# Optimization experiments

Hardware: AMD Instinct MI355X
Metric: run time of the kernel (lower is better)

Reference implementation:

```python
import jax, jax.numpy as jnp
import numpy as np

N_NODES = 1_000_000
N_UPD = 200_000
D_MEM = 172
D_MSG = 172


def setup_inputs() -> dict:
    key = jax.random.key(0)
    ks = jax.random.split(key, 8)
    memory = jax.random.normal(ks[0], (N_NODES, D_MEM), dtype=jnp.float32)
    last_update = jnp.zeros((N_NODES,), dtype=jnp.float32)
    # unique node ids (no duplicates, as guaranteed by the caller in the original code)
    unique_node_ids = jax.random.permutation(ks[1], N_NODES)[:N_UPD].astype(jnp.int64)
    unique_messages = jax.random.normal(ks[2], (N_UPD, D_MSG), dtype=jnp.float32)
    timestamps = jax.random.uniform(ks[3], (N_UPD,), dtype=jnp.float32) * 1e6
    s_ih = 1.0 / np.sqrt(D_MEM)
    weight_ih = jax.random.uniform(ks[4], (3 * D_MEM, D_MSG), jnp.float32, -s_ih, s_ih)
    weight_hh = jax.random.uniform(ks[5], (3 * D_MEM, D_MEM), jnp.float32, -s_ih, s_ih)
    bias_ih = jax.random.uniform(ks[6], (3 * D_MEM,), jnp.float32, -s_ih, s_ih)
    bias_hh = jax.random.uniform(ks[7], (3 * D_MEM,), jnp.float32, -s_ih, s_ih)
    return {
        "memory": memory,
        "last_update": last_update,
        "unique_node_ids": unique_node_ids,
        "unique_messages": unique_messages,
        "timestamps": timestamps,
        "weight_ih": weight_ih,
        "weight_hh": weight_hh,
        "bias_ih": bias_ih,
        "bias_hh": bias_hh,
    }


def _gru_cell(x, h, weight_ih, weight_hh, bias_ih, bias_hh):
    # PyTorch GRUCell, gate order: reset, update, new
    gi = x @ weight_ih.T + bias_ih          # [M, 3H]
    gh = h @ weight_hh.T + bias_hh          # [M, 3H]
    i_r, i_z, i_n = jnp.split(gi, 3, axis=-1)
    h_r, h_z, h_n = jnp.split(gh, 3, axis=-1)
    r = jax.nn.sigmoid(i_r + h_r)
    z = jax.nn.sigmoid(i_z + h_z)
    n = jnp.tanh(i_n + r * h_n)
    return n + z * (h - n)                  # (1-z)*n + z*h


def reference(memory, last_update, unique_node_ids, unique_messages, timestamps,
              weight_ih, weight_hh, bias_ih, bias_hh):
    # gather rows of the node memory for the updated nodes
    h = memory[unique_node_ids]                                   # [M, D]
    h_new = _gru_cell(unique_messages, h, weight_ih, weight_hh, bias_ih, bias_hh)
    # scatter updated rows back (ids are unique)
    updated_memory = memory.at[unique_node_ids].set(h_new)        # [N, D]
    updated_last_update = last_update.at[unique_node_ids].set(timestamps)
    # original module returns memory with the singleton middle dim restored
    return updated_memory[:, None, :], updated_last_update
```

## Files before the change

### kernel.cpp

```cpp
#include <hip/hip_runtime.h>

typedef __attribute__((ext_vector_type(8))) short short8;
typedef __attribute__((ext_vector_type(4))) float f32x4;

#define N_NODES 1000000
#define N_UPD   200000
#define D       172
#define BM      64
#define LDA     360
#define KSTEPS  11
#define NTILES  48
#define KSLICE  (NTILES*512)
#define GRU_BLOCKS (N_UPD / BM)
#define NM4 43000000
#define BPACK_USHORTS (KSTEPS*KSLICE)
#define BIAS_OFF  (BPACK_USHORTS*2)
#define MASK_OFF  (BIAS_OFF + 688*4)
#define WS_NEED   (MASK_OFF + N_NODES)

__device__ __forceinline__ unsigned short f2bf(float f) {
  union { float f; unsigned u; } v; v.f = f;
  unsigned r = v.u + 0x7FFFu + ((v.u >> 16) & 1u);
  return (unsigned short)(r >> 16);
}
__device__ __forceinline__ float bf2f(unsigned short h) {
  union { unsigned u; float f; } v; v.u = ((unsigned)h) << 16;
  return v.f;
}
__device__ __forceinline__ ushort4 f2bf4(float4 v) {
  return make_ushort4(f2bf(v.x), f2bf(v.y), f2bf(v.z), f2bf(v.w));
}

__global__ void prep_kernel(const float* __restrict__ wih, const float* __restrict__ whh,
                            const float* __restrict__ bih, const float* __restrict__ bhh,
                            unsigned short* __restrict__ Bpack, float* __restrict__ bias4,
                            uint4* __restrict__ mask16) {
  int gid = blockIdx.x * 256 + threadIdx.x;
  if (gid < 688) {
    int which = gid / 172, j = gid % 172;
    float v;
    if (which == 0)      v = bih[j]       + bhh[j];
    else if (which == 1) v = bih[172 + j] + bhh[172 + j];
    else if (which == 2) v = bih[344 + j];
    else                 v = bhh[344 + j];
    bias4[gid] = v;
  }
  if (gid < N_NODES / 16) mask16[gid] = make_uint4(0, 0, 0, 0);
  if (gid >= BPACK_USHORTS) return;
  int e  = gid & 7;
  int l  = (gid >> 3) & 63;
  int nt = (gid >> 9) % NTILES;
  int ks = gid / KSLICE;
  int k  = ks * 32 + ((l >> 4) << 3) + e;
  int c  = l & 15;
  int w  = nt / 12, tl = nt % 12;
  int gate = tl / 3, ti = tl % 3;
  int j = w * 48 + ti * 16 + c;
  float v = 0.f;
  if (j < D) {
    if (gate == 0) {
      if (k < D)        v = wih[j * D + k];
      else if (k < 2*D) v = whh[j * D + (k - D)];
    } else if (gate == 1) {
      if (k < D)        v = wih[(D + j) * D + k];
      else if (k < 2*D) v = whh[(D + j) * D + (k - D)];
    } else if (gate == 2) {
      if (k < D)        v = wih[(2*D + j) * D + k];
    } else {
      if (k >= D && k < 2*D) v = whh[(2*D + j) * D + (k - D)];
    }
  }
  Bpack[gid] = f2bf(v);
}

__global__ void mask_set_kernel(const int* __restrict__ ids, unsigned char* __restrict__ mask) {
  int i = blockIdx.x * 256 + threadIdx.x;
  if (i < N_UPD) mask[ids[i]] = 1;
}

__global__ void copy_kernel(const float4* __restrict__ mem4, const float4* __restrict__ lu4,
                            float4* __restrict__ out4, float4* __restrict__ outlu4) {
  const long NL4 = N_NODES / 4;
  long stride = (long)gridDim.x * blockDim.x;
  for (long i = (long)blockIdx.x * blockDim.x + threadIdx.x; i < NM4 + NL4; i += stride) {
    if (i < NM4) out4[i] = mem4[i];
    else         outlu4[i - NM4] = lu4[i - NM4];
  }
}

__global__ __launch_bounds__(256)
void copy_masked_kernel(const float4* __restrict__ mem4, const float* __restrict__ lu,
                        const unsigned char* __restrict__ mask,
                        float4* __restrict__ out4, float* __restrict__ outlu) {
  const unsigned stride = gridDim.x * 256;
  for (unsigned i = blockIdx.x * 256 + threadIdx.x; i < NM4; i += stride) {
    unsigned row = i / 43u;
    if (!mask[row]) out4[i] = mem4[i];
  }
  for (unsigned j = blockIdx.x * 256 + threadIdx.x; j < N_NODES; j += stride) {
    if (!mask[j]) outlu[j] = lu[j];
  }
}

__global__ __launch_bounds__(512, 4)
void gru64_kernel(const float* __restrict__ memory, const float* __restrict__ msgs,
                  const int* __restrict__ ids, const float* __restrict__ ts,
                  const unsigned short* __restrict__ Bpack, const float* __restrict__ bias4,
                  float* __restrict__ out_mem, float* __restrict__ out_lu) {
  __shared__ unsigned short At[BM * LDA];
  const int tid  = threadIdx.x;
  const int m0   = blockIdx.x * BM;
  const int wave = tid >> 6, lane = tid & 63;
  const int g = lane >> 4, c = lane & 15;
  const int wm = wave >> 2, wc = wave & 3;

  const float4* x4 = (const float4*)msgs + (size_t)m0 * 43;
  float4 xv[6], hv[6];
  #pragma unroll
  for (int i = 0; i < 6; ++i) {
    int s = tid + i * 512;
    if (i < 5 || s < 2752) xv[i] = x4[s];
  }
  #pragma unroll
  for (int i = 0; i < 6; ++i) {
    int s = tid + i * 512;
    if (i < 5 || s < 2752) {
      int row = s / 43, seg = s - row * 43;
      hv[i] = ((const float4*)(memory + (size_t)ids[m0 + row] * D))[seg];
    }
  }
  #pragma unroll
  for (int i = 0; i < 6; ++i) {
    int s = tid + i * 512;
    if (i < 5 || s < 2752) {
      int row = s / 43, seg = s - row * 43;
      *(ushort4*)&At[row * LDA + seg * 4]       = f2bf4(xv[i]);
      *(ushort4*)&At[row * LDA + 172 + seg * 4] = f2bf4(hv[i]);
    }
  }
  if (tid < BM) {
    *(uint4*)&At[tid * LDA + 344] = make_uint4(0, 0, 0, 0);
    out_lu[ids[m0 + tid]] = ts[m0 + tid];
  }
  __syncthreads();

  const int ar0 = (wm * 32 + c) * LDA;
  const int ar1 = ar0 + 16 * LDA;
  const short8* Bp = (const short8*)Bpack;

  #pragma unroll 1
  for (int ti = 0; ti < 3; ++ti) {
    if (wc == 3 && ti == 2) continue;
    const short8* bp = Bp + (size_t)((wc * 12 + ti) * 64 + lane);

    f32x4 Cr0={0,0,0,0}, Cr1={0,0,0,0};
    f32x4 Cz0={0,0,0,0}, Cz1={0,0,0,0};
    f32x4 Ci0={0,0,0,0}, Ci1={0,0,0,0};
    f32x4 Ch0={0,0,0,0}, Ch1={0,0,0,0};

    #pragma unroll 2
    for (int ks = 0; ks < KSTEPS; ++ks) {
      const short8* bk = bp + ks * 3072;
      short8 br = bk[0];
      short8 bz = bk[192];
      short8 bi = bk[384];
      short8 bh = bk[576];
      short8 a0 = *(const short8*)&At[ar0 + ks * 32 + g * 8];
      short8 a1 = *(const short8*)&At[ar1 + ks * 32 + g * 8];
      Cr0 = __builtin_amdgcn_mfma_f32_16x16x32_bf16(a0, br, Cr0, 0, 0, 0);
      Cr1 = __builtin_amdgcn_mfma_f32_16x16x32_bf16(a1, br, Cr1, 0, 0, 0);
      Cz0 = __builtin_amdgcn_mfma_f32_16x16x32_bf16(a0, bz, Cz0, 0, 0, 0);
      Cz1 = __builtin_amdgcn_mfma_f32_16x16x32_bf16(a1, bz, Cz1, 0, 0, 0);
      Ci0 = __builtin_amdgcn_mfma_f32_16x16x32_bf16(a0, bi, Ci0, 0, 0, 0);
      Ci1 = __builtin_amdgcn_mfma_f32_16x16x32_bf16(a1, bi, Ci1, 0, 0, 0);
      Ch0 = __builtin_amdgcn_mfma_f32_16x16x32_bf16(a0, bh, Ch0, 0, 0, 0);
      Ch1 = __builtin_amdgcn_mfma_f32_16x16x32_bf16(a1, bh, Ch1, 0, 0, 0);
    }

    const int j = wc * 48 + ti * 16 + c;
    if (j < D) {
      const float b_r = bias4[j];
      const float b_z = bias4[172 + j];
      const float b_i = bias4[344 + j];
      const float b_h = bias4[516 + j];
      #pragma unroll
      for (int r = 0; r < 4; ++r) {
        {
          const int row_local = wm * 32 + g * 4 + r;
          float* orow = out_mem + (size_t)ids[m0 + row_local] * D;
          float ho = bf2f(At[row_local * LDA + 172 + j]);
          float rr = 1.f / (1.f + __expf(-(Cr0[r] + b_r)));
          float zz = 1.f / (1.f + __expf(-(Cz0[r] + b_z)));
          float e2 = __expf(2.f * (Ci0[r] + b_i + rr * (Ch0[r] + b_h)));
          float nn = 1.f - 2.f / (e2 + 1.f);
          orow[j] = nn + zz * (ho - nn);
        }
        {
          const int row_local = wm * 32 + 16 + g * 4 + r;
          float* orow = out_mem + (size_t)ids[m0 + row_local] * D;
          float ho = bf2f(At[row_local * LDA + 172 + j]);
          float rr = 1.f / (1.f + __expf(-(Cr1[r] + b_r)));
          float zz = 1.f / (1.f + __expf(-(Cz1[r] + b_z)));
          float e2 = __expf(2.f * (Ci1[r] + b_i + rr * (Ch1[r] + b_h)));
          float nn = 1.f - 2.f / (e2 + 1.f);
          orow[j] = nn + zz * (ho - nn);
        }
      }
    }
  }
}

extern "C" void kernel_launch(void* const* d_in, const int* in_sizes, int n_in,
                              void* d_out, int out_size, void* d_ws, size_t ws_size,
                              hipStream_t stream) {
  const float* memory      = (const float*)d_in[0];
  const float* last_update = (const float*)d_in[1];
  const int*   ids         = (const int*)  d_in[2];
  const float* msgs        = (const float*)d_in[3];
  const float* ts          = (const float*)d_in[4];
  const float* wih         = (const float*)d_in[5];
  const float* whh         = (const float*)d_in[6];
  const float* bih         = (const float*)d_in[7];
  const float* bhh         = (const float*)d_in[8];

  float* out_mem = (float*)d_out;
  float* out_lu  = out_mem + (size_t)N_NODES * D;

  unsigned short* Bpack = (unsigned short*)d_ws;
  float* bias4 = (float*)((char*)d_ws + BIAS_OFF);
  unsigned char* mask = (unsigned char*)d_ws + MASK_OFF;

  prep_kernel<<<BPACK_USHORTS / 256, 256, 0, stream>>>(wih, whh, bih, bhh, Bpack, bias4,
                                                       (uint4*)mask);
  if (ws_size >= WS_NEED) {
    mask_set_kernel<<<(N_UPD + 255) / 256, 256, 0, stream>>>(ids, mask);
    copy_masked_kernel<<<2048, 256, 0, stream>>>((const float4*)memory, last_update, mask,
                                                 (float4*)out_mem, out_lu);
  } else {
    copy_kernel<<<4096, 256, 0, stream>>>((const float4*)memory, (const float4*)last_update,
                                          (float4*)out_mem, (float4*)out_lu);
  }
  gru64_kernel<<<GRU_BLOCKS, 512, 0, stream>>>(memory, msgs, ids, ts, Bpack, bias4,
                                               out_mem, out_lu);
}
```

Before: 492.7 us.

## Interleave packed B weights per lane, software-pipeline B loads, row-coalesced A staging

The packed weight layout is reordered so each lane's four gate fragments for a k-step sit contiguously, and the GRU kernel's k-loop is fully unrolled with a three-stage register prefetch of B fragments ahead of the MFMAs. The A-tile staging now has 8 threads per row load contiguous float4s from message and memory rows, which gives contiguous access within each gathered row. Bf16 conversion switches to the HIP library paired round-to-nearest intrinsic. The aim is to hide weight-load latency and improve gather coalescing, at the cost of more live registers under the 512x4 launch bound.

```diff
diff --git a/kernel.cpp b/kernel.cpp
--- a/kernel.cpp
+++ b/kernel.cpp
@@ -1,4 +1,5 @@
 #include <hip/hip_runtime.h>
+#include <hip/hip_bf16.h>
 
 typedef __attribute__((ext_vector_type(8))) short short8;
 typedef __attribute__((ext_vector_type(4))) float f32x4;
@@ -9,26 +10,24 @@
 #define BM      64
 #define LDA     360
 #define KSTEPS  11
-#define NTILES  48
-#define KSLICE  (NTILES*512)
+#define KSTRIDE 24576
 #define GRU_BLOCKS (N_UPD / BM)
-#define NM4 43000000
-#define BPACK_USHORTS (KSTEPS*KSLICE)
+#define NM4     43000000
+#define BPACK_USHORTS (KSTEPS*KSTRIDE)
 #define BIAS_OFF  (BPACK_USHORTS*2)
 #define MASK_OFF  (BIAS_OFF + 688*4)
 #define WS_NEED   (MASK_OFF + N_NODES)
 
-__device__ __forceinline__ unsigned short f2bf(float f) {
-  union { float f; unsigned u; } v; v.f = f;
-  unsigned r = v.u + 0x7FFFu + ((v.u >> 16) & 1u);
-  return (unsigned short)(r >> 16);
-}
 __device__ __forceinline__ float bf2f(unsigned short h) {
   union { unsigned u; float f; } v; v.u = ((unsigned)h) << 16;
   return v.f;
 }
-__device__ __forceinline__ ushort4 f2bf4(float4 v) {
-  return make_ushort4(f2bf(v.x), f2bf(v.y), f2bf(v.z), f2bf(v.w));
+__device__ __forceinline__ uint2 f2bf4p(float4 v) {
+  __hip_bfloat162 lo = __float22bfloat162_rn(make_float2(v.x, v.y));
+  __hip_bfloat162 hi = __float22bfloat162_rn(make_float2(v.z, v.w));
+  union { __hip_bfloat162 b; unsigned u; } a, b2;
+  a.b = lo; b2.b = hi;
+  return make_uint2(a.u, b2.u);
 }
 
 __global__ void prep_kernel(const float* __restrict__ wih, const float* __restrict__ whh,
@@ -47,15 +46,16 @@
   }
   if (gid < N_NODES / 16) mask16[gid] = make_uint4(0, 0, 0, 0);
   if (gid >= BPACK_USHORTS) return;
-  int e  = gid & 7;
-  int l  = (gid >> 3) & 63;
-  int nt = (gid >> 9) % NTILES;
-  int ks = gid / KSLICE;
-  int k  = ks * 32 + ((l >> 4) << 3) + e;
-  int c  = l & 15;
-  int w  = nt / 12, tl = nt % 12;
-  int gate = tl / 3, ti = tl % 3;
-  int j = w * 48 + ti * 16 + c;
+  int e    = gid & 7;
+  int gate = (gid >> 3) & 3;
+  int l    = (gid >> 5) & 63;
+  int r2   = gid >> 11;
+  int ti   = r2 % 3;
+  int wcg  = (r2 / 3) & 3;
+  int ks   = r2 / 12;
+  int k    = ks * 32 + ((l >> 4) << 3) + e;
+  int c    = l & 15;
+  int j    = wcg * 48 + ti * 16 + c;
   float v = 0.f;
   if (j < D) {
     if (gate == 0) {
@@ -70,7 +70,9 @@
       if (k >= D && k < 2*D) v = whh[(2*D + j) * D + (k - D)];
     }
   }
-  Bpack[gid] = f2bf(v);
+  union { __hip_bfloat16 b; unsigned short s; } cv;
+  cv.b = __float2bfloat16(v);
+  Bpack[gid] = cv.s;
 }
 
 __global__ void mask_set_kernel(const int* __restrict__ ids, unsigned char* __restrict__ mask) {
@@ -114,68 +116,83 @@
   const int g = lane >> 4, c = lane & 15;
   const int wm = wave >> 2, wc = wave & 3;
 
-  const float4* x4 = (const float4*)msgs + (size_t)m0 * 43;
-  float4 xv[6], hv[6];
-  #pragma unroll
-  for (int i = 0; i < 6; ++i) {
-    int s = tid + i * 512;
-    if (i < 5 || s < 2752) xv[i] = x4[s];
-  }
-  #pragma unroll
-  for (int i = 0; i < 6; ++i) {
-    int s = tid + i * 512;
-    if (i < 5 || s < 2752) {
-      int row = s / 43, seg = s - row * 43;
-      hv[i] = ((const float4*)(memory + (size_t)ids[m0 + row] * D))[seg];
-    }
-  }
-  #pragma unroll
-  for (int i = 0; i < 6; ++i) {
-    int s = tid + i * 512;
-    if (i < 5 || s < 2752) {
-      int row = s / 43, seg = s - row * 43;
-      *(ushort4*)&At[row * LDA + seg * 4]       = f2bf4(xv[i]);
-      *(ushort4*)&At[row * LDA + 172 + seg * 4] = f2bf4(hv[i]);
-    }
-  }
-  if (tid < BM) {
-    *(uint4*)&At[tid * LDA + 344] = make_uint4(0, 0, 0, 0);
-    out_lu[ids[m0 + tid]] = ts[m0 + tid];
+  {
+    const int row = tid >> 3, q = tid & 3 ? (tid & 7) : (tid & 7);
+    const int qq = tid & 7;
+    const float4* xrow = (const float4*)(msgs + (size_t)(m0 + row) * D);
+    const float4* hrow = (const float4*)(memory + (size_t)ids[m0 + row] * D);
+    float4 x0 = xrow[qq];      float4 x1 = xrow[qq + 8];
+    float4 x2 = xrow[qq + 16]; float4 x3 = xrow[qq + 24];
+    float4 x4v = xrow[qq + 32];
+    float4 h0 = hrow[qq];      float4 h1 = hrow[qq + 8];
+    float4 h2 = hrow[qq + 16]; float4 h3 = hrow[qq + 24];
+    float4 h4 = hrow[qq + 32];
+    float4 x5, h5;
+    if (qq < 3) { x5 = xrow[qq + 40]; h5 = hrow[qq + 40]; }
+    unsigned short* ar = &At[row * LDA];
+    *(uint2*)&ar[(qq    ) * 4] = f2bf4p(x0);
+    *(uint2*)&ar[(qq + 8) * 4] = f2bf4p(x1);
+    *(uint2*)&ar[(qq +16) * 4] = f2bf4p(x2);
+    *(uint2*)&ar[(qq +24) * 4] = f2bf4p(x3);
+    *(uint2*)&ar[(qq +32) * 4] = f2bf4p(x4v);
+    *(uint2*)&ar[172 + (qq    ) * 4] = f2bf4p(h0);
+    *(uint2*)&ar[172 + (qq + 8) * 4] = f2bf4p(h1);
+    *(uint2*)&ar[172 + (qq +16) * 4] = f2bf4p(h2);
+    *(uint2*)&ar[172 + (qq +24) * 4] = f2bf4p(h3);
+    *(uint2*)&ar[172 + (qq +32) * 4] = f2bf4p(h4);
+    if (qq < 3) {
+      *(uint2*)&ar[(qq + 40) * 4]       = f2bf4p(x5);
+      *(uint2*)&ar[172 + (qq + 40) * 4] = f2bf4p(h5);
+    }
+    if (tid < BM) {
+      *(uint4*)&At[tid * LDA + 344] = make_uint4(0, 0, 0, 0);
+      out_lu[ids[m0 + tid]] = ts[m0 + tid];
+    }
   }
   __syncthreads();
 
   const int ar0 = (wm * 32 + c) * LDA;
   const int ar1 = ar0 + 16 * LDA;
-  const short8* Bp = (const short8*)Bpack;
 
   #pragma unroll 1
   for (int ti = 0; ti < 3; ++ti) {
     if (wc == 3 && ti == 2) continue;
-    const short8* bp = Bp + (size_t)((wc * 12 + ti) * 64 + lane);
+    const unsigned short* bb = Bpack + ((size_t)((wc * 3 + ti) * 64 + lane)) * 32;
 
     f32x4 Cr0={0,0,0,0}, Cr1={0,0,0,0};
     f32x4 Cz0={0,0,0,0}, Cz1={0,0,0,0};
     f32x4 Ci0={0,0,0,0}, Ci1={0,0,0,0};
     f32x4 Ch0={0,0,0,0}, Ch1={0,0,0,0};
-
-    #pragma unroll 2
-    for (int ks = 0; ks < KSTEPS; ++ks) {
-      const short8* bk = bp + ks * 3072;
-      short8 br = bk[0];
-      short8 bz = bk[192];
-      short8 bi = bk[384];
-      short8 bh = bk[576];
-      short8 a0 = *(const short8*)&At[ar0 + ks * 32 + g * 8];
-      short8 a1 = *(const short8*)&At[ar1 + ks * 32 + g * 8];
-      Cr0 = __builtin_amdgcn_mfma_f32_16x16x32_bf16(a0, br, Cr0, 0, 0, 0);
-      Cr1 = __builtin_amdgcn_mfma_f32_16x16x32_bf16(a1, br, Cr1, 0, 0, 0);
-      Cz0 = __builtin_amdgcn_mfma_f32_16x16x32_bf16(a0, bz, Cz0, 0, 0, 0);
-      Cz1 = __builtin_amdgcn_mfma_f32_16x16x32_bf16(a1, bz, Cz1, 0, 0, 0);
-      Ci0 = __builtin_amdgcn_mfma_f32_16x16x32_bf16(a0, bi, Ci0, 0, 0, 0);
-      Ci1 = __builtin_amdgcn_mfma_f32_16x16x32_bf16(a1, bi, Ci1, 0, 0, 0);
-      Ch0 = __builtin_amdgcn_mfma_f32_16x16x32_bf16(a0, bh, Ch0, 0, 0, 0);
-      Ch1 = __builtin_amdgcn_mfma_f32_16x16x32_bf16(a1, bh, Ch1, 0, 0, 0);
-    }
+    short8 R0,Z0,I0,H0, R1,Z1,I1,H1, R2,Z2,I2,H2;
+
+#define LOADB(S, KS) { const short8* _b = (const short8*)(bb + (size_t)(KS) * KSTRIDE); \
+    R##S = _b[0]; Z##S = _b[1]; I##S = _b[2]; H##S = _b[3]; }
+#define DOMFMA(S, KS) { \
+    short8 a0 = *(const short8*)&At[ar0 + (KS)*32 + g*8]; \
+    short8 a1 = *(const short8*)&At[ar1 + (KS)*32 + g*8]; \
+    Cr0 = __builtin_amdgcn_mfma_f32_16x16x32_bf16(a0, R##S, Cr0, 0, 0, 0); \
+    Cr1 = __builtin_amdgcn_mfma_f32_16x16x32_bf16(a1, R##S, Cr1, 0, 0, 0); \
+    Cz0 = __builtin_amdgcn_mfma_f32_16x16x32_bf16(a0, Z##S, Cz0, 0, 0, 0); \
+    Cz1 = __builtin_amdgcn_mfma_f32_16x16x32_bf16(a1, Z##S, Cz1, 0, 0, 0); \
+    Ci0 = __builtin_amdgcn_mfma_f32_16x16x32_bf16(a0, I##S, Ci0, 0, 0, 0); \
+    Ci1 = __builtin_amdgcn_mfma_f32_16x16x32_bf16(a1, I##S, Ci1, 0, 0, 0); \
+    Ch0 = __builtin_amdgcn_mfma_f32_16x16x32_bf16(a0, H##S, Ch0, 0, 0, 0); \
+    Ch1 = __builtin_amdgcn_mfma_f32_16x16x32_bf16(a1, H##S, Ch1, 0, 0, 0); }
+
+    LOADB(0, 0)  LOADB(1, 1)
+    LOADB(2, 2)  DOMFMA(0, 0)
+    LOADB(0, 3)  DOMFMA(1, 1)
+    LOADB(1, 4)  DOMFMA(2, 2)
+    LOADB(2, 5)  DOMFMA(0, 3)
+    LOADB(0, 6)  DOMFMA(1, 4)
+    LOADB(1, 7)  DOMFMA(2, 5)
+    LOADB(2, 8)  DOMFMA(0, 6)
+    LOADB(0, 9)  DOMFMA(1, 7)
+    LOADB(1, 10) DOMFMA(2, 8)
+    DOMFMA(0, 9)
+    DOMFMA(1, 10)
+#undef LOADB
+#undef DOMFMA
 
     const int j = wc * 48 + ti * 16 + c;
     if (j < D) {
```

Result: slower. 591.3 us (+20.0%).
